# Performance work log

Measured on AMD Instinct MI355X. Metric: run time of the kernel, lower is better.

Reference implementation:

```python
import jax, jax.numpy as jnp
import numpy as np

WS = 4        # window_size
SHIFT = 3     # shift_size
HEADS = 4
DIM = 128
HR, WR = 256, 256  # input_resolution (matches post-upsample H, W)


def _rel_pos_index(ws):
    coords = np.stack(np.meshgrid(np.arange(ws), np.arange(ws), indexing='ij'))  # (2, ws, ws)
    cf = coords.reshape(2, -1)
    rel = (cf[:, :, None] - cf[:, None, :]).transpose(1, 2, 0).astype(np.int64)
    rel[:, :, 0] += ws - 1
    rel[:, :, 1] += ws - 1
    rel[:, :, 0] *= 2 * ws - 1
    return rel.sum(-1)  # (N, N)


def _attn_mask(H, W, ws, shift):
    img = np.zeros((H, W))
    cnt = 0
    sl = (slice(0, -ws), slice(-ws, -shift), slice(-shift, None))
    for hs in sl:
        for wsl in sl:
            img[hs, wsl] = cnt
            cnt += 1
    mw = img.reshape(H // ws, ws, W // ws, ws).transpose(0, 2, 1, 3).reshape(-1, ws * ws)
    diff = mw[:, None, :] - mw[:, :, None]  # unsqueeze(1) - unsqueeze(2)
    return np.where(diff != 0, -100.0, 0.0).astype(np.float32)  # (nW, N, N)


REL_IDX = jnp.asarray(_rel_pos_index(WS))
ATTN_MASK = jnp.asarray(_attn_mask(HR, WR, WS, SHIFT))


def _upsample2x_ac(x):
    def interp(x, axis):
        n = x.shape[axis]
        m = 2 * n
        pos = jnp.arange(m) * ((n - 1) / (m - 1))
        lo = jnp.floor(pos).astype(jnp.int32)
        hi = jnp.minimum(lo + 1, n - 1)
        w = (pos - lo).astype(x.dtype)
        shp = [1] * x.ndim
        shp[axis] = m
        w = w.reshape(shp)
        return jnp.take(x, lo, axis=axis) * (1 - w) + jnp.take(x, hi, axis=axis) * w
    return interp(interp(x, 2), 3)


def _conv2d(x, w, b, pad):
    y = jax.lax.conv_general_dilated(x, w, (1, 1), [(pad, pad), (pad, pad)],
                                     dimension_numbers=('NCHW', 'OIHW', 'NCHW'))
    return y + b[None, :, None, None]


def _bn(x, g, b, m, v):
    # eval-mode BatchNorm2d
    s = g / jnp.sqrt(v + 1e-5)
    return x * s[None, :, None, None] + (b - m * s)[None, :, None, None]


def setup_inputs():
    key = jax.random.key(0)
    ks = jax.random.split(key, 8)
    f = jax.random.normal
    return {
        'x': f(ks[0], (4, 256, 128, 64), jnp.float32),
        'qkv_w': f(ks[1], (DIM, 3 * DIM), jnp.float32) * 0.02,
        'qkv_b': jnp.zeros((3 * DIM,), jnp.float32),
        'proj_w': f(ks[2], (DIM, DIM), jnp.float32) * 0.02,
        'proj_b': jnp.zeros((DIM,), jnp.float32),
        'rpb': f(ks[3], ((2 * WS - 1) ** 2, HEADS), jnp.float32) * 0.02,
        'conv1_w': f(ks[4], (256, 256, 3, 3), jnp.float32) * 0.02,
        'conv1_b': jnp.zeros((256,), jnp.float32),
        'bn1_g': jnp.ones((256,), jnp.float32),
        'bn1_b': jnp.zeros((256,), jnp.float32),
        'bn1_m': jnp.zeros((256,), jnp.float32),
        'bn1_v': jnp.ones((256,), jnp.float32),
        'conv2_w': f(ks[5], (256, 256, 3, 3), jnp.float32) * 0.02,
        'conv2_b': jnp.zeros((256,), jnp.float32),
        'bn2_g': jnp.ones((256,), jnp.float32),
        'bn2_b': jnp.zeros((256,), jnp.float32),
        'bn2_m': jnp.zeros((256,), jnp.float32),
        'bn2_v': jnp.ones((256,), jnp.float32),
        'idc_w': f(ks[6], (256, 256, 1, 1), jnp.float32) * 0.02,
        'idc_b': jnp.zeros((256,), jnp.float32),
        'bni_g': jnp.ones((256,), jnp.float32),
        'bni_b': jnp.zeros((256,), jnp.float32),
        'bni_m': jnp.zeros((256,), jnp.float32),
        'bni_v': jnp.ones((256,), jnp.float32),
    }


def reference(x, qkv_w, qkv_b, proj_w, proj_b, rpb,
              conv1_w, conv1_b, bn1_g, bn1_b, bn1_m, bn1_v,
              conv2_w, conv2_b, bn2_g, bn2_b, bn2_m, bn2_v,
              idc_w, idc_b, bni_g, bni_b, bni_m, bni_v):
    x = _upsample2x_ac(x)                 # (B, 256, 256, 128), treated as (B,H,W,C) downstream
    B, H, W, C = x.shape
    shortcut = x
    xs = jnp.roll(x, (-SHIFT, -SHIFT), axis=(1, 2))
    # window partition -> (B*nW, N, C)
    nWh, nWw = H // WS, W // WS
    xw = xs.reshape(B, nWh, WS, nWw, WS, C).transpose(0, 1, 3, 2, 4, 5).reshape(-1, WS * WS, C)
    B_, N, _ = xw.shape
    hd = C // HEADS
    qkv = (xw @ qkv_w + qkv_b).reshape(B_, N, 3, HEADS, hd).transpose(2, 0, 3, 1, 4)
    q, k, v = qkv[0], qkv[1], qkv[2]
    attn = jnp.einsum('bhnd,bhmd->bhnm', q * (hd ** -0.5), k)
    bias = rpb[REL_IDX.reshape(-1)].reshape(N, N, HEADS).transpose(2, 0, 1)  # (h, N, N)
    attn = attn + bias[None]
    nW = ATTN_MASK.shape[0]
    attn = attn.reshape(B_ // nW, nW, HEADS, N, N) + ATTN_MASK[None, :, None]
    attn = jax.nn.softmax(attn.reshape(B_, HEADS, N, N), axis=-1)
    out = jnp.einsum('bhnm,bhmd->bhnd', attn, v).transpose(0, 2, 1, 3).reshape(B_, N, C)
    out = out @ proj_w + proj_b
    # window reverse + roll back
    out = out.reshape(B, nWh, nWw, WS, WS, C).transpose(0, 1, 3, 2, 4, 5).reshape(B, H, W, C)
    out = jnp.roll(out, (SHIFT, SHIFT), axis=(1, 2))
    x = shortcut + out
    # DoubleConv with identity branch (tensor treated as NCHW, per original code)
    y = _conv2d(x, conv1_w, conv1_b, 1)
    y = jax.nn.relu(_bn(y, bn1_g, bn1_b, bn1_m, bn1_v))
    y = _conv2d(y, conv2_w, conv2_b, 1)
    y = _bn(y, bn2_g, bn2_b, bn2_m, bn2_v)
    idn = _bn(_conv2d(x, idc_w, idc_b, 0), bni_g, bni_b, bni_m, bni_v)
    return jax.nn.relu(y + idn)
```

## Files before the change

### kernel.cpp

```cpp
#include <hip/hip_runtime.h>
#include <hip/hip_bf16.h>
#include <math.h>
#include <cstddef>

#define BATCH 4
#define WDIM 256
#define CDIM 128
#define WS 4
#define SHIFT 3
#define HEADS 4
#define HD 32
#define NTOK 16

typedef __attribute__((ext_vector_type(8))) short short8;
typedef __attribute__((ext_vector_type(4))) int int4v;
typedef __attribute__((ext_vector_type(4))) float f32x4;

__device__ __forceinline__ int regionOf(int v) {
    return v < (WDIM - WS) ? 0 : (v < (WDIM - SHIFT) ? 1 : 2);
}

__device__ __forceinline__ short f2bf(float v) {
    __hip_bfloat16 h = __float2bfloat16(v);
    return __builtin_bit_cast(short, h);
}
__device__ __forceinline__ float bf2f(short s) {
    unsigned u = ((unsigned)(unsigned short)s) << 16;
    return __builtin_bit_cast(float, u);
}

__global__ __launch_bounds__(256) void repack_attnw(
    const float* __restrict__ qkv_w,
    const float* __restrict__ proj_w,
    __hip_bfloat16* __restrict__ qkvw_rep,
    __hip_bfloat16* __restrict__ projw_rep)
{
    int idx = blockIdx.x * 256 + threadIdx.x;
    if (idx < 49152) {
        int j = idx >> 7, c = idx & 127;
        qkvw_rep[idx] = __float2bfloat16(qkv_w[c * 384 + j]);
    } else {
        int k = idx - 49152;
        int j = k >> 7, c = k & 127;
        projw_rep[k] = __float2bfloat16(proj_w[c * 128 + j]);
    }
}

__global__ __launch_bounds__(256, 4) void attn_kernel(
    const float* __restrict__ xin,
    const __hip_bfloat16* __restrict__ qkvw_rep,
    const __hip_bfloat16* __restrict__ projw_rep,
    const float* __restrict__ qkv_b,
    const float* __restrict__ proj_b,
    const float* __restrict__ rpb,
    __hip_bfloat16* __restrict__ xatt)
{
    __shared__ __align__(16) char smem[40848];
    float* xrowF  = (float*)smem;
    short* qkvs   = (short*)smem;
    short* aoutS  = (short*)smem;
    short* Xb     = (short*)(smem + 16896);
    short* Ps     = (short*)(smem + 25600);
    short* Vt     = (short*)(smem + 29696);
    float* rpbs   = (float*)(smem + 37888);
    float* qkvbS  = (float*)(smem + 38672);
    float* projbS = (float*)(smem + 40208);
    float* tokw2  = (float*)(smem + 40720);

    const int tid = threadIdx.x;
    const int bid = blockIdx.x;
    const int l   = tid & 63;
    const int wv  = tid >> 6;
    const int lm  = l & 15;
    const int lq  = l >> 4;

    if (tid < 196) rpbs[tid] = rpb[tid];
    for (int i = tid; i < 384; i += 256) qkvbS[i] = qkv_b[i];
    if (tid < 128) projbS[tid] = proj_b[tid];

    #pragma unroll
    for (int k = 0; k < 4; k++) {
        int id = tid + k * 256;
        int n   = id >> 5;
        int row = (id >> 4) & 1;
        int ll  = id & 15;
        int w_  = n >> 4, nn = n & 15;
        int win = bid * 2 + w_;
        int b   = win >> 12;
        int wh  = (win >> 6) & 63;
        int ww  = win & 63;
        int r = nn >> 2, c = nn & 3;
        int gh = (wh * 4 + r + SHIFT) & 255;
        int gw = (ww * 4 + c + SHIFT) & 255;
        float pos2 = gw * (127.0f / 255.0f);
        int lo2 = (int)floorf(pos2);
        int hi2 = min(lo2 + 1, 127);
        if (row == 0 && ll == 0) tokw2[n] = pos2 - (float)lo2;
        int src = row == 0 ? lo2 : hi2;
        const float4* rp = (const float4*)(xin + (((size_t)b * 256 + gh) * 128 + src) * 64);
        ((float4*)(xrowF + n * 132 + row * 64))[ll] = rp[ll];
    }
    __syncthreads();

    {
        int n = tid >> 3;
        int jj = tid & 7;
        float w2 = tokw2[n];
        const float* xr0 = xrowF + n * 132;
        const float* xr1 = xr0 + 64;
        #pragma unroll
        for (int i = 0; i < 16; i++) {
            int cc = jj * 16 + i;
            float pos3 = cc * (63.0f / 127.0f);
            int lo3 = (int)floorf(pos3);
            int hi3 = min(lo3 + 1, 63);
            float w3 = pos3 - (float)lo3;
            float v0 = xr0[lo3] * (1.f - w3) + xr0[hi3] * w3;
            float v1 = xr1[lo3] * (1.f - w3) + xr1[hi3] * w3;
            Xb[n * 136 + cc] = f2bf(v0 * (1.f - w2) + v1 * w2);
        }
    }
    __syncthreads();

    {
        f32x4 qacc[6][2];
        #pragma unroll
        for (int a = 0; a < 6; a++)
            #pragma unroll
            for (int t = 0; t < 2; t++) qacc[a][t] = (f32x4)0.0f;

        for (int ks = 0; ks < 4; ks++) {
            short8 af[6];
            #pragma unroll
            for (int jj = 0; jj < 6; jj++) {
                const int4v* gp = (const int4v*)(qkvw_rep +
                    (size_t)(wv * 96 + jj * 16 + lm) * 128 + ks * 32 + lq * 8);
                af[jj] = __builtin_bit_cast(short8, *gp);
            }
            short8 bfr[2];
            #pragma unroll
            for (int tt = 0; tt < 2; tt++)
                bfr[tt] = *(const short8*)&Xb[(tt * 16 + lm) * 136 + ks * 32 + lq * 8];
            #pragma unroll
            for (int jj = 0; jj < 6; jj++)
                #pragma unroll
                for (int tt = 0; tt < 2; tt++)
                    qacc[jj][tt] = __builtin_amdgcn_mfma_f32_16x16x32_bf16(
                        af[jj], bfr[tt], qacc[jj][tt], 0, 0, 0);
        }
        #pragma unroll
        for (int jj = 0; jj < 6; jj++) {
            int jbase = wv * 96 + jj * 16 + lq * 4;
            #pragma unroll
            for (int tt = 0; tt < 2; tt++) {
                int tok = tt * 16 + lm;
                if (jbase < 128) {
                    float v0 = (qacc[jj][tt][0] + qkvbS[jbase+0]) * 0.17677669529663687f;
                    float v1 = (qacc[jj][tt][1] + qkvbS[jbase+1]) * 0.17677669529663687f;
                    float v2 = (qacc[jj][tt][2] + qkvbS[jbase+2]) * 0.17677669529663687f;
                    float v3 = (qacc[jj][tt][3] + qkvbS[jbase+3]) * 0.17677669529663687f;
                    unsigned p0 = (unsigned short)f2bf(v0) | ((unsigned)(unsigned short)f2bf(v1) << 16);
                    unsigned p1 = (unsigned short)f2bf(v2) | ((unsigned)(unsigned short)f2bf(v3) << 16);
                    *(unsigned*)&qkvs[tok * 264 + jbase]     = p0;
                    *(unsigned*)&qkvs[tok * 264 + jbase + 2] = p1;
                } else if (jbase < 256) {
                    float v0 = qacc[jj][tt][0] + qkvbS[jbase+0];
                    float v1 = qacc[jj][tt][1] + qkvbS[jbase+1];
                    float v2 = qacc[jj][tt][2] + qkvbS[jbase+2];
                    float v3 = qacc[jj][tt][3] + qkvbS[jbase+3];
                    unsigned p0 = (unsigned short)f2bf(v0) | ((unsigned)(unsigned short)f2bf(v1) << 16);
                    unsigned p1 = (unsigned short)f2bf(v2) | ((unsigned)(unsigned short)f2bf(v3) << 16);
                    *(unsigned*)&qkvs[tok * 264 + jbase]     = p0;
                    *(unsigned*)&qkvs[tok * 264 + jbase + 2] = p1;
                } else {
                    #pragma unroll
                    for (int r = 0; r < 4; r++) {
                        int d = jbase - 256 + r;
                        Vt[(tt * 128 + d) * 16 + lm] = f2bf(qacc[jj][tt][r] + qkvbS[jbase + r]);
                    }
                }
            }
        }
    }
    __syncthreads();

    {
        int w_ = wv >> 1;
        int hb = (wv & 1) * 2;
        int win = bid * 2 + w_;
        int wh = (win >> 6) & 63;
        int ww = win & 63;
        int m  = lm;
        int r2 = m >> 2, c2 = m & 3;
        int reg2 = regionOf(wh * 4 + r2) * 3 + regionOf(ww * 4 + c2);
        #pragma unroll
        for (int hh = 0; hh < 2; hh++) {
            int h = hb + hh;
            short8 qa = *(const short8*)&qkvs[(w_ * 16 + lm) * 264 + h * 32 + lq * 8];
            short8 kb = *(const short8*)&qkvs[(w_ * 16 + lm) * 264 + 128 + h * 32 + lq * 8];
            f32x4 s = __builtin_amdgcn_mfma_f32_16x16x32_bf16(qa, kb, (f32x4)0.0f, 0, 0, 0);
            #pragma unroll
            for (int r = 0; r < 4; r++) {
                int n = lq * 4 + r;
                int r1 = n >> 2, c1 = n & 3;
                int ridx = (r1 - r2 + 3) * 7 + (c1 - c2 + 3);
                float v = s[r] + rpbs[ridx * 4 + h];
                int reg1 = regionOf(wh * 4 + r1) * 3 + regionOf(ww * 4 + c1);
                if (reg1 != reg2) v -= 100.f;
                float mx = v;
                mx = fmaxf(mx, __shfl_xor(mx, 1));
                mx = fmaxf(mx, __shfl_xor(mx, 2));
                mx = fmaxf(mx, __shfl_xor(mx, 4));
                mx = fmaxf(mx, __shfl_xor(mx, 8));
                float e = __expf(v - mx);
                float ss = e;
                ss += __shfl_xor(ss, 1);
                ss += __shfl_xor(ss, 2);
                ss += __shfl_xor(ss, 4);
                ss += __shfl_xor(ss, 8);
                Ps[((w_ * 4 + h) * 16 + n) * 16 + m] = f2bf(e / ss);
            }
        }
    }
    __syncthreads();

    {
        int w_ = wv >> 1;
        int hb = (wv & 1) * 2;
        #pragma unroll
        for (int hh = 0; hh < 2; hh++) {
            int h = hb + hh;
            #pragma unroll
            for (int dt = 0; dt < 2; dt++) {
                short8 pa = (short8)0;
                short8 vb = (short8)0;
                if (lq < 2) {
                    pa = *(const short8*)&Ps[((w_ * 4 + h) * 16 + lm) * 16 + lq * 8];
                    vb = *(const short8*)&Vt[(w_ * 128 + h * 32 + dt * 16 + lm) * 16 + lq * 8];
                }
                f32x4 o = __builtin_amdgcn_mfma_f32_16x16x32_bf16(pa, vb, (f32x4)0.0f, 0, 0, 0);
                #pragma unroll
                for (int r = 0; r < 4; r++) {
                    aoutS[(w_ * 16 + lq * 4 + r) * 136 + h * 32 + dt * 16 + lm] = f2bf(o[r]);
                }
            }
        }
    }
    __syncthreads();

    {
        f32x4 cacc[2][2];
        #pragma unroll
        for (int a = 0; a < 2; a++)
            #pragma unroll
            for (int t = 0; t < 2; t++) cacc[a][t] = (f32x4)0.0f;

        for (int ks = 0; ks < 4; ks++) {
            short8 af[2];
            #pragma unroll
            for (int jj = 0; jj < 2; jj++) {
                const int4v* gp = (const int4v*)(projw_rep +
                    (size_t)(wv * 32 + jj * 16 + lm) * 128 + ks * 32 + lq * 8);
                af[jj] = __builtin_bit_cast(short8, *gp);
            }
            short8 bfr[2];
            #pragma unroll
            for (int tt = 0; tt < 2; tt++)
                bfr[tt] = *(const short8*)&aoutS[(tt * 16 + lm) * 136 + ks * 32 + lq * 8];
            #pragma unroll
            for (int jj = 0; jj < 2; jj++)
                #pragma unroll
                for (int tt = 0; tt < 2; tt++)
                    cacc[jj][tt] = __builtin_amdgcn_mfma_f32_16x16x32_bf16(
                        af[jj], bfr[tt], cacc[jj][tt], 0, 0, 0);
        }
        __syncthreads();
        #pragma unroll
        for (int jj = 0; jj < 2; jj++) {
            int jbase = wv * 32 + jj * 16 + lq * 4;
            #pragma unroll
            for (int tt = 0; tt < 2; tt++) {
                int tok = tt * 16 + lm;
                float v0 = cacc[jj][tt][0] + projbS[jbase+0] + bf2f(Xb[tok * 136 + jbase+0]);
                float v1 = cacc[jj][tt][1] + projbS[jbase+1] + bf2f(Xb[tok * 136 + jbase+1]);
                float v2 = cacc[jj][tt][2] + projbS[jbase+2] + bf2f(Xb[tok * 136 + jbase+2]);
                float v3 = cacc[jj][tt][3] + projbS[jbase+3] + bf2f(Xb[tok * 136 + jbase+3]);
                unsigned p0 = (unsigned short)f2bf(v0) | ((unsigned)(unsigned short)f2bf(v1) << 16);
                unsigned p1 = (unsigned short)f2bf(v2) | ((unsigned)(unsigned short)f2bf(v3) << 16);
                *(unsigned*)&aoutS[tok * 136 + jbase]     = p0;
                *(unsigned*)&aoutS[tok * 136 + jbase + 2] = p1;
            }
        }
    }
    __syncthreads();

    {
        #pragma unroll
        for (int k = 0; k < 4; k++) {
            int idx = k * 256 + tid;
            int j  = idx & 127;
            int c  = (idx >> 7) & 3;
            int w_ = idx >> 9;
            int win = bid * 2 + w_;
            int b   = win >> 12;
            int wh  = (win >> 6) & 63;
            int ww  = win & 63;
            int gw  = (ww * 4 + c + SHIFT) & 255;
            int slot0 = (wh * 4 + SHIFT + 1) & 255;
            unsigned short s0 = (unsigned short)aoutS[(w_ * 16 + 0 + c) * 136 + j];
            unsigned short s1 = (unsigned short)aoutS[(w_ * 16 + 4 + c) * 136 + j];
            unsigned short s2 = (unsigned short)aoutS[(w_ * 16 + 8 + c) * 136 + j];
            unsigned short s3 = (unsigned short)aoutS[(w_ * 16 + 12 + c) * 136 + j];
            unsigned long long pk =
                (unsigned long long)s0 | ((unsigned long long)s1 << 16) |
                ((unsigned long long)s2 << 32) | ((unsigned long long)s3 << 48);
            size_t base = (((size_t)b * 256 + gw) * 128 + j) * 256 + slot0;
            *(unsigned long long*)(xatt + base) = pk;
        }
    }
}

__global__ __launch_bounds__(256) void repack3(
    const float* __restrict__ w, const float* __restrict__ bias,
    const float* __restrict__ g_, const float* __restrict__ b_,
    const float* __restrict__ m_, const float* __restrict__ v_,
    __hip_bfloat16* __restrict__ wrep, float* __restrict__ cconst, int roll)
{
    int idx = blockIdx.x * 256 + threadIdx.x;
    int co = idx / 2304;
    int rem = idx - co * 2304;
    int ci = rem / 9;
    int tap = rem - ci * 9;
    float s = g_[co] * rsqrtf(v_[co] + 1e-5f);
    int ci_s = (ci + roll) & 255;
    size_t o = ((((size_t)(co >> 7) * 8 + (ci_s >> 5)) * 9 + tap) * 128 + (co & 127)) * 32 + (ci_s & 31);
    wrep[o] = __float2bfloat16(w[idx] * s);
    if (rem == 0) cconst[co] = bias[co] * s + (b_[co] - m_[co] * s);
}

__global__ __launch_bounds__(256) void repack1(
    const float* __restrict__ w, const float* __restrict__ bias,
    const float* __restrict__ g_, const float* __restrict__ b_,
    const float* __restrict__ m_, const float* __restrict__ v_,
    __hip_bfloat16* __restrict__ wrep, float* __restrict__ cconst)
{
    int idx = blockIdx.x * 256 + threadIdx.x;
    int co = idx >> 8, ci = idx & 255;
    float s = g_[co] * rsqrtf(v_[co] + 1e-5f);
    int ci_s = (ci + 1) & 255;
    wrep[(((size_t)(co >> 7) * 8 + (ci_s >> 5)) * 128 + (co & 127)) * 32 + (ci_s & 31)] =
        __float2bfloat16(w[idx] * s);
    if (ci == 0) cconst[co] += bias[co] * s + (b_[co] - m_[co] * s);
}

template<int HAS_IDC, int OUT_BF16>
__global__ __launch_bounds__(256) void conv_mfma(
    const __hip_bfloat16* __restrict__ xin,
    const __hip_bfloat16* __restrict__ xidc,
    const __hip_bfloat16* __restrict__ wrep,
    const __hip_bfloat16* __restrict__ wrepi,
    const float* __restrict__ cconst,
    void* __restrict__ outp)
{
    constexpr int NROWS = HAS_IDC ? 4 : 3;
    constexpr int NPER  = NROWS * 2;
    constexpr int NTAPS = HAS_IDC ? 10 : 9;
    __shared__ __align__(16) short xs[NROWS * 130 * 40];

    const int tid = threadIdx.x;
    const int l  = tid & 63;
    const int wv = tid >> 6;
    const int wave_co = (wv & 1) * 64;
    const int wave_w  = (wv >> 1) * 64;
    const int g = blockIdx.x & 1;
    const int h = (blockIdx.x >> 1) & 255;
    const int n = blockIdx.x >> 9;
    const int lq = l >> 4;
    const int lm = l & 15;

    if (tid < 192) {
        int row = tid >> 6;
        int side = (tid >> 5) & 1;
        int ci = tid & 31;
        xs[(row * 130 + (side ? 129 : 0)) * 40 + ci] = 0;
    }

    f32x4 acc[4][4];
    #pragma unroll
    for (int a = 0; a < 4; a++)
        #pragma unroll
        for (int b = 0; b < 4; b++) acc[a][b] = (f32x4)0.0f;

    int4v pre[NPER];
    #pragma unroll
    for (int t = 0; t < NPER; t++) {
        int idx = t * 256 + tid;
        int c8  = idx & 3;
        int w   = (idx >> 2) & 127;
        int row = idx >> 9;
        int4v v = {0, 0, 0, 0};
        if (row < 3) {
            int hh = h - 1 + row;
            if (0 <= hh && hh < 256)
                v = *(const int4v*)(xin + ((((size_t)n * 256 + hh) * 128 + w) << 8) + c8 * 8);
        } else {
            v = *(const int4v*)(xidc + ((((size_t)n * 256 + h) * 128 + w) << 8) + c8 * 8);
        }
        pre[t] = v;
    }

    #pragma unroll 1
    for (int cb = 0; cb < 8; cb++) {
        __syncthreads();
        #pragma unroll
        for (int t = 0; t < NPER; t++) {
            int idx = t * 256 + tid;
            int c8  = idx & 3;
            int w   = (idx >> 2) & 127;
            int row = idx >> 9;
            *(int4v*)&xs[(row * 130 + w + 1) * 40 + c8 * 8] = pre[t];
        }
        __syncthreads();
        if (cb < 7) {
            #pragma unroll
            for (int t = 0; t < NPER; t++) {
                int idx = t * 256 + tid;
                int c8  = idx & 3;
                int w   = (idx >> 2) & 127;
                int row = idx >> 9;
                int4v v = {0, 0, 0, 0};
                if (row < 3) {
                    int hh = h - 1 + row;
                    if (0 <= hh && hh < 256)
                        v = *(const int4v*)(xin + ((((size_t)n * 256 + hh) * 128 + w) << 8)
                                            + (cb + 1) * 32 + c8 * 8);
                } else {
                    v = *(const int4v*)(xidc + ((((size_t)n * 256 + h) * 128 + w) << 8)
                                        + (cb + 1) * 32 + c8 * 8);
                }
                pre[t] = v;
            }
        }

        #pragma unroll 1
        for (int tap = 0; tap < NTAPS; tap++) {
            const __hip_bfloat16* ap;
            const short* bs;
            if (tap < 9) {
                int kh = tap / 3;
                int kw = tap - kh * 3;
                ap = wrep + ((((size_t)(g * 8 + cb) * 9 + tap)) << 12);
                bs = xs + (kh * 130 + wave_w + kw) * 40;
            } else {
                ap = wrepi + (((size_t)(g * 8 + cb)) << 12);
                bs = xs + (3 * 130 + wave_w + 1) * 40;
            }
            short8 afr[4];
            #pragma unroll
            for (int cs = 0; cs < 4; cs++) {
                const int4v* p4 = (const int4v*)(ap + (size_t)(wave_co + cs * 16 + lm) * 32 + lq * 8);
                afr[cs] = __builtin_bit_cast(short8, *p4);
            }
            #pragma unroll
            for (int ws = 0; ws < 4; ws++) {
                short8 bfr = __builtin_bit_cast(short8,
                    *(const int4v*)&bs[(ws * 16 + lm) * 40 + lq * 8]);
                #pragma unroll
                for (int cs = 0; cs < 4; cs++) {
                    acc[cs][ws] = __builtin_amdgcn_mfma_f32_16x16x32_bf16(
                        afr[cs], bfr, acc[cs][ws], 0, 0, 0);
                }
            }
        }
    }

    #pragma unroll
    for (int cs = 0; cs < 4; cs++) {
        int co0 = g * 128 + wave_co + cs * 16 + lq * 4;
        float c0 = cconst[co0 + 0], c1 = cconst[co0 + 1];
        float c2 = cconst[co0 + 2], c3 = cconst[co0 + 3];
        #pragma unroll
        for (int ws = 0; ws < 4; ws++) {
            int w = wave_w + ws * 16 + lm;
            float v0 = fmaxf(acc[cs][ws][0] + c0, 0.f);
            float v1 = fmaxf(acc[cs][ws][1] + c1, 0.f);
            float v2 = fmaxf(acc[cs][ws][2] + c2, 0.f);
            float v3 = fmaxf(acc[cs][ws][3] + c3, 0.f);
            if (OUT_BF16) {
                unsigned long long pk =
                    (unsigned long long)(unsigned short)f2bf(v0) |
                    ((unsigned long long)(unsigned short)f2bf(v1) << 16) |
                    ((unsigned long long)(unsigned short)f2bf(v2) << 32) |
                    ((unsigned long long)(unsigned short)f2bf(v3) << 48);
                size_t base = ((((size_t)n * 256 + h) * 128 + w) << 8) + co0;
                *(unsigned long long*)((__hip_bfloat16*)outp + base) = pk;
            } else {
                float* op = (float*)outp;
                op[(((size_t)n * 256 + co0 + 0) * 256 + h) * 128 + w] = v0;
                op[(((size_t)n * 256 + co0 + 1) * 256 + h) * 128 + w] = v1;
                op[(((size_t)n * 256 + co0 + 2) * 256 + h) * 128 + w] = v2;
                op[(((size_t)n * 256 + co0 + 3) * 256 + h) * 128 + w] = v3;
            }
        }
    }
}

extern "C" void kernel_launch(void* const* d_in, const int* in_sizes, int n_in,
                              void* d_out, int out_size, void* d_ws, size_t ws_size,
                              hipStream_t stream) {
    const float* x       = (const float*)d_in[0];
    const float* qkv_w   = (const float*)d_in[1];
    const float* qkv_b   = (const float*)d_in[2];
    const float* proj_w  = (const float*)d_in[3];
    const float* proj_b  = (const float*)d_in[4];
    const float* rpb     = (const float*)d_in[5];
    const float* conv1_w = (const float*)d_in[6];
    const float* conv1_b = (const float*)d_in[7];
    const float* bn1_g   = (const float*)d_in[8];
    const float* bn1_b   = (const float*)d_in[9];
    const float* bn1_m   = (const float*)d_in[10];
    const float* bn1_v   = (const float*)d_in[11];
    const float* conv2_w = (const float*)d_in[12];
    const float* conv2_b = (const float*)d_in[13];
    const float* bn2_g   = (const float*)d_in[14];
    const float* bn2_b   = (const float*)d_in[15];
    const float* bn2_m   = (const float*)d_in[16];
    const float* bn2_v   = (const float*)d_in[17];
    const float* idc_w   = (const float*)d_in[18];
    const float* idc_b   = (const float*)d_in[19];
    const float* bni_g   = (const float*)d_in[20];
    const float* bni_b   = (const float*)d_in[21];
    const float* bni_m   = (const float*)d_in[22];
    const float* bni_v   = (const float*)d_in[23];

    const size_t TE = (size_t)BATCH * 256 * 256 * 128;
    char* ws = (char*)d_ws;
    __hip_bfloat16* xatt  = (__hip_bfloat16*)(ws);
    __hip_bfloat16* y1    = (__hip_bfloat16*)(ws + TE * 2);
    __hip_bfloat16* wrep1 = (__hip_bfloat16*)(ws + TE * 4);
    __hip_bfloat16* wrep2 = (__hip_bfloat16*)(ws + TE * 4 + 1179648);
    __hip_bfloat16* wrepi = (__hip_bfloat16*)(ws + TE * 4 + 2359296);
    float*          c1    = (float*)(ws + TE * 4 + 2490368);
    float*          c2    = (float*)(ws + TE * 4 + 2491392);
    __hip_bfloat16* qkvw_rep = (__hip_bfloat16*)(ws + TE * 4 + 2492416);
    __hip_bfloat16* projw_rep= (__hip_bfloat16*)(ws + TE * 4 + 2590720);

    repack3<<<2304, 256, 0, stream>>>(conv1_w, conv1_b, bn1_g, bn1_b, bn1_m, bn1_v, wrep1, c1, 1);
    repack3<<<2304, 256, 0, stream>>>(conv2_w, conv2_b, bn2_g, bn2_b, bn2_m, bn2_v, wrep2, c2, 0);
    repack1<<<256, 256, 0, stream>>>(idc_w, idc_b, bni_g, bni_b, bni_m, bni_v, wrepi, c2);
    repack_attnw<<<256, 256, 0, stream>>>(qkv_w, proj_w, qkvw_rep, projw_rep);

    attn_kernel<<<8192, 256, 0, stream>>>(x, qkvw_rep, projw_rep, qkv_b, proj_b, rpb, xatt);

    conv_mfma<0, 1><<<2048, 256, 0, stream>>>(xatt, nullptr, wrep1, nullptr, c1, (void*)y1);
    conv_mfma<1, 0><<<2048, 256, 0, stream>>>(y1, xatt, wrep2, wrepi, c2, d_out);
}
```

Before: 774.3 us.

## Double-buffer conv weight fragments, read identity input directly, remap block order

The conv MFMA kernel now prefetches the next tap's weight fragments into a second register buffer while the current tap's MFMAs run, so global weight load latency overlaps compute. The identity-conv input row is read straight from global memory into registers instead of being staged in shared memory, which cuts LDS use to three rows and drops one prefetch slice. The kernel also sets a minimum of 4 blocks per CU in its launch bounds and remaps block indices to interleave work across the grid. The extra fragment buffers raise register pressure, and the occupancy hint may cause spills.

```diff
diff --git a/kernel.cpp b/kernel.cpp
--- a/kernel.cpp
+++ b/kernel.cpp
@@ -354,7 +354,7 @@
 }
 
 template<int HAS_IDC, int OUT_BF16>
-__global__ __launch_bounds__(256) void conv_mfma(
+__global__ __launch_bounds__(256, 4) void conv_mfma(
     const __hip_bfloat16* __restrict__ xin,
     const __hip_bfloat16* __restrict__ xidc,
     const __hip_bfloat16* __restrict__ wrep,
@@ -362,19 +362,19 @@
     const float* __restrict__ cconst,
     void* __restrict__ outp)
 {
-    constexpr int NROWS = HAS_IDC ? 4 : 3;
-    constexpr int NPER  = NROWS * 2;
+    constexpr int NPER  = 6;
     constexpr int NTAPS = HAS_IDC ? 10 : 9;
-    __shared__ __align__(16) short xs[NROWS * 130 * 40];
+    __shared__ __align__(16) short xs[3 * 130 * 40];
 
     const int tid = threadIdx.x;
     const int l  = tid & 63;
     const int wv = tid >> 6;
     const int wave_co = (wv & 1) * 64;
     const int wave_w  = (wv >> 1) * 64;
-    const int g = blockIdx.x & 1;
-    const int h = (blockIdx.x >> 1) & 255;
-    const int n = blockIdx.x >> 9;
+    const int nb = ((blockIdx.x & 7) << 8) | (blockIdx.x >> 3);
+    const int g = nb & 1;
+    const int h = (nb >> 1) & 255;
+    const int n = nb >> 9;
     const int lq = l >> 4;
     const int lm = l & 15;
 
@@ -399,13 +399,9 @@
         int w   = (idx >> 2) & 127;
         int row = idx >> 9;
         int4v v = {0, 0, 0, 0};
-        if (row < 3) {
-            int hh = h - 1 + row;
-            if (0 <= hh && hh < 256)
-                v = *(const int4v*)(xin + ((((size_t)n * 256 + hh) * 128 + w) << 8) + c8 * 8);
-        } else {
-            v = *(const int4v*)(xidc + ((((size_t)n * 256 + h) * 128 + w) << 8) + c8 * 8);
-        }
+        int hh = h - 1 + row;
+        if (0 <= hh && hh < 256)
+            v = *(const int4v*)(xin + ((((size_t)n * 256 + hh) * 128 + w) << 8) + c8 * 8);
         pre[t] = v;
     }
 
@@ -421,6 +417,50 @@
             *(int4v*)&xs[(row * 130 + w + 1) * 40 + c8 * 8] = pre[t];
         }
         __syncthreads();
+
+        short8 afrA[4], afrB[4], vb9[4];
+        auto loadW = [&](int tap, short8* afr) {
+            const __hip_bfloat16* ap = (!HAS_IDC || tap < 9)
+                ? wrep + ((((size_t)(g * 8 + cb) * 9 + tap)) << 12)
+                : wrepi + (((size_t)(g * 8 + cb)) << 12);
+            #pragma unroll
+            for (int cs = 0; cs < 4; cs++)
+                afr[cs] = __builtin_bit_cast(short8,
+                    *(const int4v*)(ap + (size_t)(wave_co + cs * 16 + lm) * 32 + lq * 8));
+            if (HAS_IDC && tap == 9) {
+                const __hip_bfloat16* bp = xidc + ((((size_t)n * 256 + h) * 128) << 8) + cb * 32;
+                #pragma unroll
+                for (int ws = 0; ws < 4; ws++)
+                    vb9[ws] = __builtin_bit_cast(short8,
+                        *(const int4v*)(bp + (size_t)(wave_w + ws * 16 + lm) * 256 + lq * 8));
+            }
+        };
+        auto computeT = [&](int tap, short8* afr) {
+            if (HAS_IDC && tap == 9) {
+                #pragma unroll
+                for (int ws = 0; ws < 4; ws++)
+                    #pragma unroll
+                    for (int cs = 0; cs < 4; cs++)
+                        acc[cs][ws] = __builtin_amdgcn_mfma_f32_16x16x32_bf16(
+                            afr[cs], vb9[ws], acc[cs][ws], 0, 0, 0);
+            } else {
+                int kh = tap / 3, kw = tap - kh * 3;
+                const short* bs = xs + (kh * 130 + wave_w + kw) * 40;
+                #pragma unroll
+                for (int ws = 0; ws < 4; ws++) {
+                    short8 bfr = __builtin_bit_cast(short8,
+                        *(const int4v*)&bs[(ws * 16 + lm) * 40 + lq * 8]);
+                    #pragma unroll
+                    for (int cs = 0; cs < 4; cs++)
+                        acc[cs][ws] = __builtin_amdgcn_mfma_f32_16x16x32_bf16(
+                            afr[cs], bfr, acc[cs][ws], 0, 0, 0);
+                }
+            }
+        };
+
+        loadW(0, afrA);
+        loadW(1, afrB);
+
         if (cb < 7) {
             #pragma unroll
             for (int t = 0; t < NPER; t++) {
@@ -429,47 +469,22 @@
                 int w   = (idx >> 2) & 127;
                 int row = idx >> 9;
                 int4v v = {0, 0, 0, 0};
-                if (row < 3) {
-                    int hh = h - 1 + row;
-                    if (0 <= hh && hh < 256)
-                        v = *(const int4v*)(xin + ((((size_t)n * 256 + hh) * 128 + w) << 8)
-                                            + (cb + 1) * 32 + c8 * 8);
-                } else {
-                    v = *(const int4v*)(xidc + ((((size_t)n * 256 + h) * 128 + w) << 8)
+                int hh = h - 1 + row;
+                if (0 <= hh && hh < 256)
+                    v = *(const int4v*)(xin + ((((size_t)n * 256 + hh) * 128 + w) << 8)
                                         + (cb + 1) * 32 + c8 * 8);
-                }
                 pre[t] = v;
             }
         }
 
+        computeT(0, afrA);
         #pragma unroll 1
-        for (int tap = 0; tap < NTAPS; tap++) {
-            const __hip_bfloat16* ap;
-            const short* bs;
-            if (tap < 9) {
-                int kh = tap / 3;
-                int kw = tap - kh * 3;
-                ap = wrep + ((((size_t)(g * 8 + cb) * 9 + tap)) << 12);
-                bs = xs + (kh * 130 + wave_w + kw) * 40;
-            } else {
-                ap = wrepi + (((size_t)(g * 8 + cb)) << 12);
-                bs = xs + (3 * 130 + wave_w + 1) * 40;
-            }
-            short8 afr[4];
-            #pragma unroll
-            for (int cs = 0; cs < 4; cs++) {
-                const int4v* p4 = (const int4v*)(ap + (size_t)(wave_co + cs * 16 + lm) * 32 + lq * 8);
-                afr[cs] = __builtin_bit_cast(short8, *p4);
-            }
-            #pragma unroll
-            for (int ws = 0; ws < 4; ws++) {
-                short8 bfr = __builtin_bit_cast(short8,
-                    *(const int4v*)&bs[(ws * 16 + lm) * 40 + lq * 8]);
-                #pragma unroll
-                for (int cs = 0; cs < 4; cs++) {
-                    acc[cs][ws] = __builtin_amdgcn_mfma_f32_16x16x32_bf16(
-                        afr[cs], bfr, acc[cs][ws], 0, 0, 0);
-                }
+        for (int tap = 1; tap < NTAPS; tap += 2) {
+            if (tap + 1 < NTAPS) loadW(tap + 1, afrA);
+            computeT(tap, afrB);
+            if (tap + 1 < NTAPS) {
+                if (tap + 2 < NTAPS) loadW(tap + 2, afrB);
+                computeT(tap + 1, afrA);
             }
         }
     }
```

Measured after the change: 2.564 ms. 231% more time.
